# Kernel tuning notes

Measured on AMD Instinct MI355X. Metric: run time of the kernel, lower is better.

Reference implementation:

```python
import jax, jax.numpy as jnp
import numpy as np

B, SQ, SK, H, NH = 2, 2048, 2048, 2048, 16
HD = H // NH  # 128
NEG = -1e9


def setup_inputs() -> dict:
    key = jax.random.key(0)
    ks = jax.random.split(key, 8)
    hidden_states = jax.random.normal(ks[0], (B, SQ, H), dtype=jnp.float32)
    # key already transposed/expanded for baddbmm: [B*nh, head_dim, key_len]
    k = jax.random.normal(ks[1], (B * NH, HD, SK), dtype=jnp.float32)
    v = jax.random.normal(ks[2], (B, NH, SK, HD), dtype=jnp.float32)
    # additive float causal mask [B, 1, Sq, Sk]
    causal = jnp.tril(jnp.ones((SQ, SK), dtype=bool))
    attention_mask = jnp.where(causal, 0.0, NEG).astype(jnp.float32)
    attention_mask = jnp.broadcast_to(attention_mask[None, None], (B, 1, SQ, SK))
    w_q = jax.random.normal(ks[3], (H, H), dtype=jnp.float32) * 0.02
    b_q = jnp.zeros((H,), dtype=jnp.float32)
    w_proj = jax.random.normal(ks[4], (H, H), dtype=jnp.float32) * 0.02
    b_proj = jnp.zeros((H,), dtype=jnp.float32)
    return {
        "hidden_states": hidden_states,
        "key": k,
        "value": v,
        "attention_mask": attention_mask,
        "w_q": w_q,
        "b_q": b_q,
        "w_proj": w_proj,
        "b_proj": b_proj,
    }


def reference(hidden_states, key, value, attention_mask, w_q, b_q, w_proj, b_proj):
    dtype = hidden_states.dtype
    scale = 1.0 / (HD ** 0.5)  # scale_attn_weights=True, attention_multiplier=None
    # q projection: [B, Sq, H] -> [B, nh, Sq, hd]
    q = hidden_states @ w_q.T + b_q
    q = q.reshape(B, SQ, NH, HD).transpose(0, 2, 1, 3)
    # key comes in as [B*nh, hd, Sk]
    k = key.reshape(B, NH, HD, SK)
    # scores = mask + scale * q @ k  (baddbmm with beta=1)
    scores = attention_mask + scale * jnp.einsum("bhqd,bhdk->bhqk", q, k)
    # softmax in fp32 (attention_softmax_in_fp32=True), cast back
    probs = jax.nn.softmax(scores.astype(jnp.float32), axis=-1).astype(dtype)
    # attn_pdrop=0 -> no dropout
    out = jnp.einsum("bhqk,bhkd->bhqd", probs, value)  # [B, nh, Sq, hd]
    out = out.transpose(0, 2, 1, 3).reshape(B, SQ, H)
    out = out @ w_proj.T + b_proj  # resid_pdrop=0 -> no dropout
    return out
```

## Files before the change

### kernel.cpp

```cpp
#include <hip/hip_runtime.h>
#include <hip/hip_bf16.h>

typedef __bf16 bf16;
typedef __bf16 bf16x4 __attribute__((ext_vector_type(4)));
typedef __bf16 bf16x8 __attribute__((ext_vector_type(8)));
typedef float  f32x4  __attribute__((ext_vector_type(4)));
typedef unsigned int u32;

#define B_   2
#define SQ_  2048
#define SK_  2048
#define H_   2048
#define NH_  16
#define HD_  128
#define BH_  (B_*NH_)

__device__ inline void gl_lds16(const bf16* g, bf16* l) {
  __builtin_amdgcn_global_load_lds(
      (const __attribute__((address_space(1))) u32*)(const void*)g,
      (__attribute__((address_space(3))) u32*)(void*)l,
      16, 0, 0);
}

__device__ inline float exp2_fast(float x) {
  float r; asm("v_exp_f32 %0, %1" : "=v"(r) : "v"(x)); return r;
}

__global__ __launch_bounds__(256) void cvt3_f32_bf16(const float* __restrict__ a, bf16* __restrict__ ao,
                                                     const float* __restrict__ b, bf16* __restrict__ bo,
                                                     const float* __restrict__ c, bf16* __restrict__ co) {
  const int blk = blockIdx.x;
  const float* in; bf16* out; int n4, bstart, nblk;
  if (blk < 1024)      { in = a; out = ao; n4 = (B_ * SQ_ * H_) / 4; bstart = 0;    nblk = 1024; }
  else if (blk < 1536) { in = b; out = bo; n4 = (H_ * H_) / 4;       bstart = 1024; nblk = 512; }
  else                 { in = c; out = co; n4 = (H_ * H_) / 4;       bstart = 1536; nblk = 512; }
  int i = (blk - bstart) * 256 + threadIdx.x;
  const int stride = nblk * 256;
  for (; i < n4; i += stride) {
    float4 v = ((const float4*)in)[i];
    bf16x4 w; w[0] = (bf16)v.x; w[1] = (bf16)v.y; w[2] = (bf16)v.z; w[3] = (bf16)v.w;
    ((bf16x4*)out)[i] = w;
  }
}

__global__ __launch_bounds__(256) void transpose_cvt2(const float* __restrict__ key,
                                                      const float* __restrict__ value,
                                                      bf16* __restrict__ kout,
                                                      bf16* __restrict__ vout) {
  __shared__ float tile[64][65];
  const int id = blockIdx.x;
  const float* src; bf16* dst; int R, C, r0, c0, bh;
  if (id < 2048) {
    src = key; dst = kout; R = HD_; C = SK_;
    c0 = (id & 31) * 64; r0 = ((id >> 5) & 1) * 64; bh = id >> 6;
  } else {
    const int j = id - 2048;
    src = value; dst = vout; R = SK_; C = HD_;
    c0 = (j & 1) * 64; r0 = ((j >> 1) & 31) * 64; bh = j >> 6;
  }
  src += (size_t)bh * R * C;
  dst += (size_t)bh * R * C;
  const int t = threadIdx.x;
  const int tx = t & 15, ty = t >> 4;
#pragma unroll
  for (int p = 0; p < 4; ++p) {
    int rr = ty + p * 16;
    float4 v = *(const float4*)&src[(size_t)(r0 + rr) * C + c0 + tx * 4];
    tile[rr][tx * 4 + 0] = v.x; tile[rr][tx * 4 + 1] = v.y;
    tile[rr][tx * 4 + 2] = v.z; tile[rr][tx * 4 + 3] = v.w;
  }
  __syncthreads();
#pragma unroll
  for (int p = 0; p < 4; ++p) {
    int cc = ty + p * 16;
    bf16x4 w;
#pragma unroll
    for (int i = 0; i < 4; ++i) w[i] = (bf16)tile[tx * 4 + i][cc];
    *(bf16x4*)&dst[(size_t)(c0 + cc) * R + r0 + tx * 4] = w;
  }
}

template <typename OutT>
__global__ __launch_bounds__(256) void gemm_bt(const bf16* __restrict__ A,
                                               const bf16* __restrict__ Bw,
                                               const float* __restrict__ bias,
                                               OutT* __restrict__ C,
                                               int M, int N, int K, float osc) {
  __shared__ bf16 Abuf[128 * 32];
  __shared__ bf16 Bbuf[128 * 32];
  const int nbn = N >> 7;
  int wg = blockIdx.x, nwg = gridDim.x;
  int swz = (nwg & 7) ? wg : ((wg & 7) * (nwg >> 3) + (wg >> 3));
  int bm = swz / nbn, bn = swz % nbn;
  const int t = threadIdx.x, lane = t & 63, wid = t >> 6;
  const int r = lane & 15, g = lane >> 4;
  const int wr = wid >> 1, wc = wid & 1;
  const size_t m0 = (size_t)bm * 128, n0 = (size_t)bn * 128;

  f32x4 acc[4][4];
#pragma unroll
  for (int m = 0; m < 4; ++m)
#pragma unroll
    for (int n = 0; n < 4; ++n) acc[m][n] = (f32x4){0.f, 0.f, 0.f, 0.f};

  for (int k0 = 0; k0 < K; k0 += 32) {
    __syncthreads();
#pragma unroll
    for (int p = 0; p < 2; ++p) {
      int c = p * 256 + t;
      int row = c >> 2, off = c & 3;
      gl_lds16(A + (m0 + row) * K + k0 + off * 8, &Abuf[(p * 256 + wid * 64) * 8]);
      gl_lds16(Bw + (n0 + row) * K + k0 + off * 8, &Bbuf[(p * 256 + wid * 64) * 8]);
    }
    __syncthreads();
    bf16x8 af[4], bfr[4];
#pragma unroll
    for (int m = 0; m < 4; ++m)
      af[m] = *(const bf16x8*)&Abuf[(wr * 64 + m * 16 + r) * 32 + g * 8];
#pragma unroll
    for (int n = 0; n < 4; ++n)
      bfr[n] = *(const bf16x8*)&Bbuf[(wc * 64 + n * 16 + r) * 32 + g * 8];
#pragma unroll
    for (int m = 0; m < 4; ++m)
#pragma unroll
      for (int n = 0; n < 4; ++n)
        acc[m][n] = __builtin_amdgcn_mfma_f32_16x16x32_bf16(af[m], bfr[n], acc[m][n], 0, 0, 0);
  }

  float bv[4];
#pragma unroll
  for (int n = 0; n < 4; ++n) bv[n] = bias[n0 + wc * 64 + n * 16 + r];
#pragma unroll
  for (int m = 0; m < 4; ++m)
#pragma unroll
    for (int n = 0; n < 4; ++n)
#pragma unroll
      for (int rr = 0; rr < 4; ++rr) {
        size_t row = m0 + wr * 64 + m * 16 + g * 4 + rr;
        size_t col = n0 + wc * 64 + n * 16 + r;
        C[row * N + col] = (OutT)((acc[m][n][rr] + bv[n]) * osc);
      }
}

__device__ __forceinline__ void softmax_prep(const f32x4 (&s)[4], bool diag,
                                             int r, int g, int qrow_base, int s_base,
                                             float (&mrun)[4], float (&lpart)[4],
                                             f32x4 (&acc)[8], bf16* pldsw,
                                             bf16x8 (&pa)[2]) {
  float sv[4][4];
#pragma unroll
  for (int sb = 0; sb < 4; ++sb)
#pragma unroll
    for (int rr = 0; rr < 4; ++rr) {
      float x = s[sb][rr];
      if (diag && (s_base + sb * 16 + r > qrow_base + g * 4 + rr)) x = -3.0e38f;
      sv[sb][rr] = x;
    }
  float pm[4];
  bool cond = true;
#pragma unroll
  for (int rr = 0; rr < 4; ++rr) {
    pm[rr] = fmaxf(fmaxf(sv[0][rr], sv[1][rr]), fmaxf(sv[2][rr], sv[3][rr]));
    cond = cond && (pm[rr] <= mrun[rr] + 10.0f);
  }
  if (!__all(cond ? 1 : 0)) {
    f32x4 corrv;
#pragma unroll
    for (int rr = 0; rr < 4; ++rr) {
      float mx = pm[rr];
#pragma unroll
      for (int d = 1; d < 16; d <<= 1) mx = fmaxf(mx, __shfl_xor(mx, d));
      float mnew = fmaxf(mrun[rr], mx);
      float corr = exp2_fast(mrun[rr] - mnew);
      mrun[rr] = mnew;
      lpart[rr] *= corr;
      corrv[rr] = corr;
    }
#pragma unroll
    for (int nb = 0; nb < 8; ++nb) acc[nb] *= corrv;
  }
#pragma unroll
  for (int sb = 0; sb < 4; ++sb)
#pragma unroll
    for (int rr = 0; rr < 4; ++rr) {
      float p = exp2_fast(sv[sb][rr] - mrun[rr]);
      lpart[rr] += p;
      pldsw[(g * 4 + rr) * 68 + sb * 16 + r] = (bf16)p;
    }
#pragma unroll
  for (int k2 = 0; k2 < 2; ++k2)
    pa[k2] = *(const bf16x8*)&pldsw[r * 68 + k2 * 32 + g * 8];
}

__global__ __launch_bounds__(256, 2) void flash_attn(const bf16* __restrict__ Q,
                                                     const bf16* __restrict__ Kt,
                                                     const bf16* __restrict__ Vt,
                                                     bf16* __restrict__ O,
                                                     bf16* __restrict__ part,
                                                     float2* __restrict__ mlbuf) {
  __shared__ bf16 Klds[2][64 * 128];
  __shared__ bf16 Vlds[2][128 * 64];
  __shared__ bf16 Plds[4][16 * 68];

  const int id = blockIdx.x;
  const int pr = (id >> 3) & 7;
  const int hf = (id >> 6) & 1;
  const int bh = (id & 7) + 8 * (id >> 7);
  const int qtA = 15 - pr, qtB = pr;
  const int nA = 2 * qtA + 2, nB = 2 * qtB + 2;
  const int b = bh >> 4, h = bh & 15;
  const int t = threadIdx.x, lane = t & 63, wid = t >> 6;
  const int r = lane & 15, g = lane >> 4;

  const bf16* Kbase = Kt + (size_t)bh * SK_ * HD_;
  const bf16* Vbase = Vt + (size_t)bh * HD_ * SK_;
  bf16* pldsw = &Plds[wid][0];

  u32 kSrc[4], vSrc[4];
#pragma unroll
  for (int p = 0; p < 4; ++p) {
    int c = p * 256 + t;
    { int row = c >> 4, off = c & 15, src = off ^ (row & 7);
      kSrc[p] = (u32)(row * HD_ + src * 8); }
    { int row = c >> 3, off = c & 7, src = off ^ (row & 7);
      vSrc[p] = (u32)(row * SK_ + src * 8); }
  }

  int cur = 0;
  const int npass = hf ? 2 : 1;
#pragma unroll 1
  for (int ps = 0; ps < npass; ++ps) {
    int qt, lo, hi, partial;
    if (!hf)          { qt = qtA; lo = 0;  hi = 17; partial = 1; }
    else if (ps == 0) { qt = qtA; lo = 17; hi = nA; partial = 1; }
    else              { qt = qtB; lo = 0;  hi = nB; partial = 0; }
    const int wb = qt * 128 + wid * 32;

    bf16x8 qf[2][4];
#pragma unroll
    for (int m = 0; m < 2; ++m) {
      const size_t qrow = ((size_t)(b * SQ_ + wb + m * 16 + r)) * H_ + (size_t)h * HD_;
#pragma unroll
      for (int kk = 0; kk < 4; ++kk)
        qf[m][kk] = *(const bf16x8*)&Q[qrow + kk * 32 + g * 8];
    }

    f32x4 acc[2][8];
    float mrun[2][4], lpart[2][4];
#pragma unroll
    for (int m = 0; m < 2; ++m) {
#pragma unroll
      for (int i = 0; i < 8; ++i) acc[m][i] = (f32x4){0.f, 0.f, 0.f, 0.f};
#pragma unroll
      for (int i = 0; i < 4; ++i) { mrun[m][i] = -3.0e38f; lpart[m][i] = 0.f; }
    }

    {
      const size_t ks = (size_t)lo * (64 * HD_), vs = (size_t)lo * 64;
#pragma unroll
      for (int p = 0; p < 4; ++p) {
        gl_lds16(Kbase + ks + kSrc[p], &Klds[cur][(p * 256 + wid * 64) * 8]);
        gl_lds16(Vbase + vs + vSrc[p], &Vlds[cur][(p * 256 + wid * 64) * 8]);
      }
    }
    asm volatile("s_waitcnt vmcnt(0)" ::: "memory");
    __syncthreads();

#pragma unroll 1
    for (int st = lo; st < hi; ++st) {
      if (st + 1 < hi) {
        const size_t ks = (size_t)(st + 1) * (64 * HD_), vs = (size_t)(st + 1) * 64;
#pragma unroll
        for (int p = 0; p < 4; ++p) {
          gl_lds16(Kbase + ks + kSrc[p], &Klds[cur ^ 1][(p * 256 + wid * 64) * 8]);
          gl_lds16(Vbase + vs + vSrc[p], &Vlds[cur ^ 1][(p * 256 + wid * 64) * 8]);
        }
      }
      const int s0 = st * 64;
      const bool act1 = (s0 <= wb + 31);
      const bool act0 = (s0 <= wb + 15);

      if (act1) {
        f32x4 sA[2][4];
#pragma unroll
        for (int m = 0; m < 2; ++m)
#pragma unroll
          for (int sb = 0; sb < 4; ++sb) sA[m][sb] = (f32x4){0.f, 0.f, 0.f, 0.f};
        __builtin_amdgcn_s_setprio(1);
        if (act0) {
#pragma unroll
          for (int sb = 0; sb < 4; ++sb) {
            const int srow = sb * 16 + r;
#pragma unroll
            for (int kk = 0; kk < 4; ++kk) {
              bf16x8 kf = *(const bf16x8*)&Klds[cur][srow * 128 + (((kk * 4 + g) ^ (srow & 7)) * 8)];
              sA[0][sb] = __builtin_amdgcn_mfma_f32_16x16x32_bf16(qf[0][kk], kf, sA[0][sb], 0, 0, 0);
              sA[1][sb] = __builtin_amdgcn_mfma_f32_16x16x32_bf16(qf[1][kk], kf, sA[1][sb], 0, 0, 0);
            }
          }
        } else {
#pragma unroll
          for (int sb = 0; sb < 4; ++sb) {
            const int srow = sb * 16 + r;
#pragma unroll
            for (int kk = 0; kk < 4; ++kk) {
              bf16x8 kf = *(const bf16x8*)&Klds[cur][srow * 128 + (((kk * 4 + g) ^ (srow & 7)) * 8)];
              sA[1][sb] = __builtin_amdgcn_mfma_f32_16x16x32_bf16(qf[1][kk], kf, sA[1][sb], 0, 0, 0);
            }
          }
        }
        __builtin_amdgcn_s_setprio(0);

        bf16x8 paf[2][2];
        if (act0)
          softmax_prep(sA[0], s0 + 63 > wb, r, g, wb, s0,
                       mrun[0], lpart[0], acc[0], pldsw, paf[0]);
        softmax_prep(sA[1], s0 + 63 > wb + 16, r, g, wb + 16, s0,
                     mrun[1], lpart[1], acc[1], pldsw, paf[1]);

        __builtin_amdgcn_s_setprio(1);
        if (act0) {
#pragma unroll
          for (int nb = 0; nb < 8; ++nb) {
            const int drow = nb * 16 + r;
#pragma unroll
            for (int k2 = 0; k2 < 2; ++k2) {
              bf16x8 vf = *(const bf16x8*)&Vlds[cur][drow * 64 + (((k2 * 4 + g) ^ (drow & 7)) * 8)];
              acc[0][nb] = __builtin_amdgcn_mfma_f32_16x16x32_bf16(paf[0][k2], vf, acc[0][nb], 0, 0, 0);
              acc[1][nb] = __builtin_amdgcn_mfma_f32_16x16x32_bf16(paf[1][k2], vf, acc[1][nb], 0, 0, 0);
            }
          }
        } else {
#pragma unroll
          for (int nb = 0; nb < 8; ++nb) {
            const int drow = nb * 16 + r;
#pragma unroll
            for (int k2 = 0; k2 < 2; ++k2) {
              bf16x8 vf = *(const bf16x8*)&Vlds[cur][drow * 64 + (((k2 * 4 + g) ^ (drow & 7)) * 8)];
              acc[1][nb] = __builtin_amdgcn_mfma_f32_16x16x32_bf16(paf[1][k2], vf, acc[1][nb], 0, 0, 0);
            }
          }
        }
        __builtin_amdgcn_s_setprio(0);
      }

      asm volatile("s_waitcnt vmcnt(0)" ::: "memory");
      __syncthreads();
      cur ^= 1;
    }

    if (partial) {
      const int slot = (hf * 8 + pr) * 32 + bh;
      bf16* pbase = part + (size_t)slot * (128 * 128);
#pragma unroll
      for (int m = 0; m < 2; ++m) {
        float lred[4];
#pragma unroll
        for (int rr = 0; rr < 4; ++rr) {
          float la = lpart[m][rr];
#pragma unroll
          for (int d = 1; d < 16; d <<= 1) la += __shfl_xor(la, d);
          lred[rr] = la;
        }
#pragma unroll
        for (int nb = 0; nb < 8; ++nb)
#pragma unroll
          for (int rr = 0; rr < 4; ++rr) {
            int row = wid * 32 + m * 16 + g * 4 + rr;
            pbase[row * 128 + nb * 16 + r] = (bf16)acc[m][nb][rr];
          }
        if (r == 0) {
#pragma unroll
          for (int rr = 0; rr < 4; ++rr) {
            int row = wid * 32 + m * 16 + g * 4 + rr;
            mlbuf[(size_t)slot * 128 + row] = float2{mrun[m][rr], lred[rr]};
          }
        }
      }
    } else {
#pragma unroll
      for (int m = 0; m < 2; ++m) {
        float inv[4];
#pragma unroll
        for (int rr = 0; rr < 4; ++rr) {
          float la = lpart[m][rr];
#pragma unroll
          for (int d = 1; d < 16; d <<= 1) la += __shfl_xor(la, d);
          inv[rr] = 1.0f / la;
        }
#pragma unroll
        for (int nb = 0; nb < 8; ++nb)
#pragma unroll
          for (int rr = 0; rr < 4; ++rr) {
            size_t row = (size_t)(b * SQ_ + wb + m * 16 + g * 4 + rr);
            O[row * H_ + (size_t)h * HD_ + nb * 16 + r] = (bf16)(acc[m][nb][rr] * inv[rr]);
          }
      }
    }
  }
}

__global__ __launch_bounds__(256) void flash_merge(const bf16* __restrict__ part,
                                                   const float2* __restrict__ mlbuf,
                                                   bf16* __restrict__ O) {
  const int idx = blockIdx.x * 2 + (threadIdx.x >> 7);
  const int d = threadIdx.x & 127;
  const int row = idx & 127;
  const int bh = (idx >> 7) & 31;
  const int pr = idx >> 12;
  const int qtA = 15 - pr;
  const int b = bh >> 4, h = bh & 15;
  const int slot0 = pr * 32 + bh;
  const int slot1 = (8 + pr) * 32 + bh;
  const float2 ml0 = mlbuf[(size_t)slot0 * 128 + row];
  const float2 ml1 = mlbuf[(size_t)slot1 * 128 + row];
  const float M = fmaxf(ml0.x, ml1.x);
  const float c0 = exp2_fast(ml0.x - M);
  const float c1 = exp2_fast(ml1.x - M);
  const float inv = 1.0f / (c0 * ml0.y + c1 * ml1.y);
  const float a0 = (float)part[(size_t)slot0 * (128 * 128) + row * 128 + d];
  const float a1 = (float)part[(size_t)slot1 * (128 * 128) + row * 128 + d];
  const size_t orow = (size_t)(b * SQ_ + qtA * 128 + row);
  O[orow * H_ + (size_t)h * HD_ + d] = (bf16)((c0 * a0 + c1 * a1) * inv);
}

extern "C" void kernel_launch(void* const* d_in, const int* in_sizes, int n_in,
                              void* d_out, int out_size, void* d_ws, size_t ws_size,
                              hipStream_t stream) {
  const float* hidden = (const float*)d_in[0];
  const float* key    = (const float*)d_in[1];
  const float* value  = (const float*)d_in[2];
  const float* w_q    = (const float*)d_in[4];
  const float* b_q    = (const float*)d_in[5];
  const float* w_proj = (const float*)d_in[6];
  const float* b_proj = (const float*)d_in[7];
  float* out = (float*)d_out;

  const size_t N_HID = (size_t)B_ * SQ_ * H_;
  const size_t N_W   = (size_t)H_ * H_;
  const size_t N_KV  = (size_t)BH_ * SK_ * HD_;
  const float SC2 = 0.08838834764831845f * 1.4426950408889634f;

  bf16* hid_bf  = (bf16*)d_ws;
  bf16* wq_bf   = hid_bf + N_HID;
  bf16* wp_bf   = wq_bf + N_W;
  bf16* k_bf    = wp_bf + N_W;
  bf16* vt_bf   = k_bf + N_KV;
  bf16* q_bf    = vt_bf + N_KV;
  bf16* part_bf = q_bf + N_HID;
  float2* ml_bf = (float2*)(part_bf + (size_t)512 * 128 * 128);
  bf16* attn_bf = hid_bf;

  cvt3_f32_bf16<<<2048, 256, 0, stream>>>(hidden, hid_bf, w_q, wq_bf, w_proj, wp_bf);
  transpose_cvt2<<<4096, 256, 0, stream>>>(key, value, k_bf, vt_bf);

  gemm_bt<bf16><<<(B_ * SQ_ / 128) * (H_ / 128), 256, 0, stream>>>(
      hid_bf, wq_bf, b_q, q_bf, B_ * SQ_, H_, H_, SC2);

  flash_attn<<<512, 256, 0, stream>>>(q_bf, k_bf, vt_bf, attn_bf, part_bf, ml_bf);
  flash_merge<<<16384, 256, 0, stream>>>(part_bf, ml_bf, attn_bf);

  gemm_bt<float><<<(B_ * SQ_ / 128) * (H_ / 128), 256, 0, stream>>>(
      attn_bf, wp_bf, b_proj, out, B_ * SQ_, H_, H_, 1.0f);
}
```

Baseline: 224.9 us.

## Switch flash attention to 32x32x16 MFMA with transposed S and register-only P

Rewrites the attention inner loop to use 32x32x16 bf16 MFMA instructions and computes S transposed (K as the A operand), so each lane owns one query row. Row max and sum then need only a single cross-half shuffle, and the P tile is converted to the PV operand layout with lane shuffles instead of a round trip through LDS. This removes the per-wave P LDS buffer and the per-row 16-lane shuffle reductions, and uses fewer, larger MFMAs. In exchange it drops the half-tile skip for the first 16 rows, so diagonal tiles compute more masked work, and it adds ds_bpermute calls to broadcast the correction and normalisation factors.

```diff
diff --git a/kernel.cpp b/kernel.cpp
--- a/kernel.cpp
+++ b/kernel.cpp
@@ -5,6 +5,7 @@
 typedef __bf16 bf16x4 __attribute__((ext_vector_type(4)));
 typedef __bf16 bf16x8 __attribute__((ext_vector_type(8)));
 typedef float  f32x4  __attribute__((ext_vector_type(4)));
+typedef float  f32x16 __attribute__((ext_vector_type(16)));
 typedef unsigned int u32;
 
 #define B_   2
@@ -25,6 +26,8 @@
 __device__ inline float exp2_fast(float x) {
   float r; asm("v_exp_f32 %0, %1" : "=v"(r) : "v"(x)); return r;
 }
+
+union PW { u32 w[4]; bf16x8 v; };
 
 __global__ __launch_bounds__(256) void cvt3_f32_bf16(const float* __restrict__ a, bf16* __restrict__ ao,
                                                      const float* __restrict__ b, bf16* __restrict__ bo,
@@ -142,56 +145,6 @@
       }
 }
 
-__device__ __forceinline__ void softmax_prep(const f32x4 (&s)[4], bool diag,
-                                             int r, int g, int qrow_base, int s_base,
-                                             float (&mrun)[4], float (&lpart)[4],
-                                             f32x4 (&acc)[8], bf16* pldsw,
-                                             bf16x8 (&pa)[2]) {
-  float sv[4][4];
-#pragma unroll
-  for (int sb = 0; sb < 4; ++sb)
-#pragma unroll
-    for (int rr = 0; rr < 4; ++rr) {
-      float x = s[sb][rr];
-      if (diag && (s_base + sb * 16 + r > qrow_base + g * 4 + rr)) x = -3.0e38f;
-      sv[sb][rr] = x;
-    }
-  float pm[4];
-  bool cond = true;
-#pragma unroll
-  for (int rr = 0; rr < 4; ++rr) {
-    pm[rr] = fmaxf(fmaxf(sv[0][rr], sv[1][rr]), fmaxf(sv[2][rr], sv[3][rr]));
-    cond = cond && (pm[rr] <= mrun[rr] + 10.0f);
-  }
-  if (!__all(cond ? 1 : 0)) {
-    f32x4 corrv;
-#pragma unroll
-    for (int rr = 0; rr < 4; ++rr) {
-      float mx = pm[rr];
-#pragma unroll
-      for (int d = 1; d < 16; d <<= 1) mx = fmaxf(mx, __shfl_xor(mx, d));
-      float mnew = fmaxf(mrun[rr], mx);
-      float corr = exp2_fast(mrun[rr] - mnew);
-      mrun[rr] = mnew;
-      lpart[rr] *= corr;
-      corrv[rr] = corr;
-    }
-#pragma unroll
-    for (int nb = 0; nb < 8; ++nb) acc[nb] *= corrv;
-  }
-#pragma unroll
-  for (int sb = 0; sb < 4; ++sb)
-#pragma unroll
-    for (int rr = 0; rr < 4; ++rr) {
-      float p = exp2_fast(sv[sb][rr] - mrun[rr]);
-      lpart[rr] += p;
-      pldsw[(g * 4 + rr) * 68 + sb * 16 + r] = (bf16)p;
-    }
-#pragma unroll
-  for (int k2 = 0; k2 < 2; ++k2)
-    pa[k2] = *(const bf16x8*)&pldsw[r * 68 + k2 * 32 + g * 8];
-}
-
 __global__ __launch_bounds__(256, 2) void flash_attn(const bf16* __restrict__ Q,
                                                      const bf16* __restrict__ Kt,
                                                      const bf16* __restrict__ Vt,
@@ -200,7 +153,6 @@
                                                      float2* __restrict__ mlbuf) {
   __shared__ bf16 Klds[2][64 * 128];
   __shared__ bf16 Vlds[2][128 * 64];
-  __shared__ bf16 Plds[4][16 * 68];
 
   const int id = blockIdx.x;
   const int pr = (id >> 3) & 7;
@@ -210,11 +162,10 @@
   const int nA = 2 * qtA + 2, nB = 2 * qtB + 2;
   const int b = bh >> 4, h = bh & 15;
   const int t = threadIdx.x, lane = t & 63, wid = t >> 6;
-  const int r = lane & 15, g = lane >> 4;
+  const int l5 = lane & 31, hiL = lane >> 5;
 
   const bf16* Kbase = Kt + (size_t)bh * SK_ * HD_;
   const bf16* Vbase = Vt + (size_t)bh * HD_ * SK_;
-  bf16* pldsw = &Plds[wid][0];
 
   u32 kSrc[4], vSrc[4];
 #pragma unroll
@@ -234,26 +185,23 @@
     if (!hf)          { qt = qtA; lo = 0;  hi = 17; partial = 1; }
     else if (ps == 0) { qt = qtA; lo = 17; hi = nA; partial = 1; }
     else              { qt = qtB; lo = 0;  hi = nB; partial = 0; }
-    const int wb = qt * 128 + wid * 32;
-
-    bf16x8 qf[2][4];
-#pragma unroll
-    for (int m = 0; m < 2; ++m) {
-      const size_t qrow = ((size_t)(b * SQ_ + wb + m * 16 + r)) * H_ + (size_t)h * HD_;
-#pragma unroll
-      for (int kk = 0; kk < 4; ++kk)
-        qf[m][kk] = *(const bf16x8*)&Q[qrow + kk * 32 + g * 8];
+    const int qbw = qt * 128 + wid * 32;
+    const int q_lane = qbw + l5;
+
+    bf16x8 qf[8];
+    {
+      const size_t qrow = (size_t)(b * SQ_ + q_lane) * H_ + (size_t)h * HD_;
+#pragma unroll
+      for (int dt = 0; dt < 8; ++dt)
+        qf[dt] = *(const bf16x8*)&Q[qrow + dt * 16 + 8 * hiL];
     }
 
-    f32x4 acc[2][8];
-    float mrun[2][4], lpart[2][4];
-#pragma unroll
-    for (int m = 0; m < 2; ++m) {
-#pragma unroll
-      for (int i = 0; i < 8; ++i) acc[m][i] = (f32x4){0.f, 0.f, 0.f, 0.f};
-#pragma unroll
-      for (int i = 0; i < 4; ++i) { mrun[m][i] = -3.0e38f; lpart[m][i] = 0.f; }
-    }
+    f32x16 acc[4];
+#pragma unroll
+    for (int n = 0; n < 4; ++n)
+#pragma unroll
+      for (int e = 0; e < 16; ++e) acc[n][e] = 0.f;
+    float mrun = -3.0e38f, lpart = 0.f;
 
     {
       const size_t ks = (size_t)lo * (64 * HD_), vs = (size_t)lo * 64;
@@ -277,68 +225,93 @@
         }
       }
       const int s0 = st * 64;
-      const bool act1 = (s0 <= wb + 31);
-      const bool act0 = (s0 <= wb + 15);
-
-      if (act1) {
-        f32x4 sA[2][4];
-#pragma unroll
-        for (int m = 0; m < 2; ++m)
-#pragma unroll
-          for (int sb = 0; sb < 4; ++sb) sA[m][sb] = (f32x4){0.f, 0.f, 0.f, 0.f};
+
+      if (s0 <= qbw + 31) {
+        f32x16 sv0, sv1;
+#pragma unroll
+        for (int e = 0; e < 16; ++e) { sv0[e] = 0.f; sv1[e] = 0.f; }
         __builtin_amdgcn_s_setprio(1);
-        if (act0) {
-#pragma unroll
-          for (int sb = 0; sb < 4; ++sb) {
-            const int srow = sb * 16 + r;
-#pragma unroll
-            for (int kk = 0; kk < 4; ++kk) {
-              bf16x8 kf = *(const bf16x8*)&Klds[cur][srow * 128 + (((kk * 4 + g) ^ (srow & 7)) * 8)];
-              sA[0][sb] = __builtin_amdgcn_mfma_f32_16x16x32_bf16(qf[0][kk], kf, sA[0][sb], 0, 0, 0);
-              sA[1][sb] = __builtin_amdgcn_mfma_f32_16x16x32_bf16(qf[1][kk], kf, sA[1][sb], 0, 0, 0);
-            }
+#pragma unroll
+        for (int dt = 0; dt < 8; ++dt) {
+          const int dch = ((2 * dt + hiL) ^ (l5 & 7)) * 8;
+          bf16x8 kf0 = *(const bf16x8*)&Klds[cur][l5 * 128 + dch];
+          bf16x8 kf1 = *(const bf16x8*)&Klds[cur][(32 + l5) * 128 + dch];
+          sv0 = __builtin_amdgcn_mfma_f32_32x32x16_bf16(kf0, qf[dt], sv0, 0, 0, 0);
+          sv1 = __builtin_amdgcn_mfma_f32_32x32x16_bf16(kf1, qf[dt], sv1, 0, 0, 0);
+        }
+        __builtin_amdgcn_s_setprio(0);
+
+        if (s0 + 63 > qbw) {
+#pragma unroll
+          for (int r2 = 0; r2 < 16; ++r2) {
+            const int kl = (r2 & 3) + 8 * (r2 >> 2) + 4 * hiL;
+            if (s0 + kl > q_lane)      sv0[r2] = -3.0e38f;
+            if (s0 + 32 + kl > q_lane) sv1[r2] = -3.0e38f;
           }
-        } else {
-#pragma unroll
-          for (int sb = 0; sb < 4; ++sb) {
-            const int srow = sb * 16 + r;
-#pragma unroll
-            for (int kk = 0; kk < 4; ++kk) {
-              bf16x8 kf = *(const bf16x8*)&Klds[cur][srow * 128 + (((kk * 4 + g) ^ (srow & 7)) * 8)];
-              sA[1][sb] = __builtin_amdgcn_mfma_f32_16x16x32_bf16(qf[1][kk], kf, sA[1][sb], 0, 0, 0);
-            }
+        }
+
+        float pm = -3.0e38f;
+#pragma unroll
+        for (int r2 = 0; r2 < 16; ++r2) pm = fmaxf(pm, fmaxf(sv0[r2], sv1[r2]));
+        pm = fmaxf(pm, __shfl_xor(pm, 32));
+        if (!__all(pm <= mrun + 10.0f ? 1 : 0)) {
+          const float mnew = fmaxf(mrun, pm);
+          const float corr = exp2_fast(mrun - mnew);
+          mrun = mnew;
+          lpart *= corr;
+          const int cb = __float_as_int(corr);
+#pragma unroll
+          for (int r2 = 0; r2 < 16; ++r2) {
+            const int q2 = (r2 & 3) + 8 * (r2 >> 2) + 4 * hiL;
+            const float cc = __int_as_float(__builtin_amdgcn_ds_bpermute(q2 * 4, cb));
+#pragma unroll
+            for (int n = 0; n < 4; ++n) acc[n][r2] *= cc;
           }
         }
-        __builtin_amdgcn_s_setprio(0);
-
-        bf16x8 paf[2][2];
-        if (act0)
-          softmax_prep(sA[0], s0 + 63 > wb, r, g, wb, s0,
-                       mrun[0], lpart[0], acc[0], pldsw, paf[0]);
-        softmax_prep(sA[1], s0 + 63 > wb + 16, r, g, wb + 16, s0,
-                     mrun[1], lpart[1], acc[1], pldsw, paf[1]);
+
+        float psum = 0.f;
+#pragma unroll
+        for (int r2 = 0; r2 < 16; ++r2) {
+          sv0[r2] = exp2_fast(sv0[r2] - mrun); psum += sv0[r2];
+          sv1[r2] = exp2_fast(sv1[r2] - mrun); psum += sv1[r2];
+        }
+        lpart += psum;
+
+        bf16x8 pa[4];
+#pragma unroll
+        for (int h2 = 0; h2 < 2; ++h2) {
+          u32 pk[8], px[8];
+#pragma unroll
+          for (int j = 0; j < 8; ++j) {
+            union { bf16 hh[2]; u32 u; } tt;
+            float plo = h2 ? sv1[2 * j] : sv0[2 * j];
+            float phi = h2 ? sv1[2 * j + 1] : sv0[2 * j + 1];
+            tt.hh[0] = (bf16)plo; tt.hh[1] = (bf16)phi;
+            pk[j] = tt.u;
+          }
+#pragma unroll
+          for (int j = 0; j < 8; ++j) px[j] = (u32)__shfl_xor((int)pk[j], 32);
+          PW a0, a1;
+          a0.w[0] = hiL ? px[2] : pk[0];
+          a0.w[1] = hiL ? px[3] : pk[1];
+          a0.w[2] = hiL ? pk[2] : px[0];
+          a0.w[3] = hiL ? pk[3] : px[1];
+          a1.w[0] = hiL ? px[6] : pk[4];
+          a1.w[1] = hiL ? px[7] : pk[5];
+          a1.w[2] = hiL ? pk[6] : px[4];
+          a1.w[3] = hiL ? pk[7] : px[5];
+          pa[2 * h2]     = a0.v;
+          pa[2 * h2 + 1] = a1.v;
+        }
 
         __builtin_amdgcn_s_setprio(1);
-        if (act0) {
-#pragma unroll
-          for (int nb = 0; nb < 8; ++nb) {
-            const int drow = nb * 16 + r;
-#pragma unroll
-            for (int k2 = 0; k2 < 2; ++k2) {
-              bf16x8 vf = *(const bf16x8*)&Vlds[cur][drow * 64 + (((k2 * 4 + g) ^ (drow & 7)) * 8)];
-              acc[0][nb] = __builtin_amdgcn_mfma_f32_16x16x32_bf16(paf[0][k2], vf, acc[0][nb], 0, 0, 0);
-              acc[1][nb] = __builtin_amdgcn_mfma_f32_16x16x32_bf16(paf[1][k2], vf, acc[1][nb], 0, 0, 0);
-            }
-          }
-        } else {
-#pragma unroll
-          for (int nb = 0; nb < 8; ++nb) {
-            const int drow = nb * 16 + r;
-#pragma unroll
-            for (int k2 = 0; k2 < 2; ++k2) {
-              bf16x8 vf = *(const bf16x8*)&Vlds[cur][drow * 64 + (((k2 * 4 + g) ^ (drow & 7)) * 8)];
-              acc[1][nb] = __builtin_amdgcn_mfma_f32_16x16x32_bf16(paf[1][k2], vf, acc[1][nb], 0, 0, 0);
-            }
+#pragma unroll
+        for (int n = 0; n < 4; ++n) {
+#pragma unroll
+          for (int kt = 0; kt < 4; ++kt) {
+            bf16x8 vf = *(const bf16x8*)&Vlds[cur][(n * 32 + l5) * 64 +
+                                                   (((2 * kt + hiL) ^ (l5 & 7)) * 8)];
+            acc[n] = __builtin_amdgcn_mfma_f32_32x32x16_bf16(pa[kt], vf, acc[n], 0, 0, 0);
           }
         }
         __builtin_amdgcn_s_setprio(0);
@@ -349,52 +322,30 @@
       cur ^= 1;
     }
 
+    float ltot = lpart + __shfl_xor(lpart, 32);
     if (partial) {
       const int slot = (hf * 8 + pr) * 32 + bh;
       bf16* pbase = part + (size_t)slot * (128 * 128);
 #pragma unroll
-      for (int m = 0; m < 2; ++m) {
-        float lred[4];
-#pragma unroll
-        for (int rr = 0; rr < 4; ++rr) {
-          float la = lpart[m][rr];
-#pragma unroll
-          for (int d = 1; d < 16; d <<= 1) la += __shfl_xor(la, d);
-          lred[rr] = la;
-        }
-#pragma unroll
-        for (int nb = 0; nb < 8; ++nb)
-#pragma unroll
-          for (int rr = 0; rr < 4; ++rr) {
-            int row = wid * 32 + m * 16 + g * 4 + rr;
-            pbase[row * 128 + nb * 16 + r] = (bf16)acc[m][nb][rr];
-          }
-        if (r == 0) {
-#pragma unroll
-          for (int rr = 0; rr < 4; ++rr) {
-            int row = wid * 32 + m * 16 + g * 4 + rr;
-            mlbuf[(size_t)slot * 128 + row] = float2{mrun[m][rr], lred[rr]};
-          }
-        }
-      }
+      for (int n = 0; n < 4; ++n)
+#pragma unroll
+        for (int r2 = 0; r2 < 16; ++r2) {
+          const int rowt = wid * 32 + (r2 & 3) + 8 * (r2 >> 2) + 4 * hiL;
+          pbase[rowt * 128 + n * 32 + l5] = (bf16)acc[n][r2];
+        }
+      if (lane < 32)
+        mlbuf[(size_t)slot * 128 + wid * 32 + lane] = float2{mrun, ltot};
     } else {
-#pragma unroll
-      for (int m = 0; m < 2; ++m) {
-        float inv[4];
-#pragma unroll
-        for (int rr = 0; rr < 4; ++rr) {
-          float la = lpart[m][rr];
-#pragma unroll
-          for (int d = 1; d < 16; d <<= 1) la += __shfl_xor(la, d);
-          inv[rr] = 1.0f / la;
-        }
-#pragma unroll
-        for (int nb = 0; nb < 8; ++nb)
-#pragma unroll
-          for (int rr = 0; rr < 4; ++rr) {
-            size_t row = (size_t)(b * SQ_ + wb + m * 16 + g * 4 + rr);
-            O[row * H_ + (size_t)h * HD_ + nb * 16 + r] = (bf16)(acc[m][nb][rr] * inv[rr]);
-          }
+      const float inv = 1.0f / ltot;
+      const int ib = __float_as_int(inv);
+#pragma unroll
+      for (int r2 = 0; r2 < 16; ++r2) {
+        const int q2 = (r2 & 3) + 8 * (r2 >> 2) + 4 * hiL;
+        const float ic = __int_as_float(__builtin_amdgcn_ds_bpermute(q2 * 4, ib));
+        const size_t rowg = (size_t)(b * SQ_ + qbw + q2);
+#pragma unroll
+        for (int n = 0; n < 4; ++n)
+          O[rowg * H_ + (size_t)h * HD_ + n * 32 + l5] = (bf16)(acc[n][r2] * ic);
       }
     }
   }
```

Result: faster. 215.6 us (-4.2%).
